# Optimization experiments

Measured on AMD Instinct MI355X. Metric: run time of the kernel, lower is better.

The kernel has to match this reference:

```python
import jax, jax.numpy as jnp
import numpy as np


def setup_inputs() -> dict:
    key = jax.random.key(0)
    k1, k2 = jax.random.split(key)
    B, D, K = 8192, 4096, 16
    x = jax.random.normal(k1, (B, D), dtype=jnp.float32)
    # kaiming_uniform_(a=sqrt(5)) on [K, D]: bound = sqrt(6/((1+5)*fan_in)) = 1/sqrt(D)
    bound = 1.0 / np.sqrt(D)
    w = jax.random.uniform(k2, (K, D), dtype=jnp.float32, minval=-bound, maxval=bound)
    return {"x": x, "w": w}


def reference(x, w):
    # z[b,d] = x[b,d] * (1 + sum_{i=1..k} w[i-1,d] * x[b,(d+i) mod D])
    k = w.shape[0]
    acc = jnp.ones_like(x)
    for i in range(1, k + 1):
        acc = acc + w[i - 1][None, :] * jnp.roll(x, -i, axis=1)
    return x * acc
```

## Files before the change

kernel.cpp:

```cpp
#include <hip/hip_runtime.h>


#define D 4096
#define DG 1024
#define K 16
#define TPB 256
#define RPB 16

typedef float f32x4 __attribute__((ext_vector_type(4)));

__global__ __launch_bounds__(TPB) void quad_enhancer_kernel(
    const float* __restrict__ x, const float* __restrict__ w,
    float* __restrict__ out) {
  const int tid = threadIdx.x;
  const int cg = blockIdx.x * TPB + tid;
  const int b0 = blockIdx.y * RPB;

  const float4* __restrict__ x4 = (const float4*)x;
  const float4* __restrict__ w4 = (const float4*)w;
  f32x4* __restrict__ o4 = (f32x4*)out;

  const int g1 = (cg + 1) & (DG - 1);
  const int g2 = (cg + 2) & (DG - 1);
  const int g3 = (cg + 3) & (DG - 1);
  const int g4 = (cg + 4) & (DG - 1);

  float4 wv[K];
#pragma unroll
  for (int i = 0; i < K; ++i) wv[i] = w4[i * DG + cg];
#pragma unroll
  for (int i = 0; i < K; ++i) {
    asm volatile("" : "+v"(wv[i].x), "+v"(wv[i].y), "+v"(wv[i].z),
                      "+v"(wv[i].w));
  }

  auto loadrow = [&](int r, float4* buf) {
    const float4* __restrict__ xr = x4 + (size_t)(b0 + r) * DG;
    buf[0] = xr[cg];
    buf[1] = xr[g1];
    buf[2] = xr[g2];
    buf[3] = xr[g3];
    buf[4] = xr[g4];
  };

  auto compute_store = [&](int r, const float4* buf) {
    float xs[20];
#pragma unroll
    for (int j = 0; j < 5; ++j) {
      xs[4 * j + 0] = buf[j].x;
      xs[4 * j + 1] = buf[j].y;
      xs[4 * j + 2] = buf[j].z;
      xs[4 * j + 3] = buf[j].w;
    }
    float ax = 1.0f, ay = 1.0f, az = 1.0f, aw = 1.0f;
#pragma unroll
    for (int i = 0; i < K; ++i) {
      ax = fmaf(wv[i].x, xs[i + 1], ax);
      ay = fmaf(wv[i].y, xs[i + 2], ay);
      az = fmaf(wv[i].z, xs[i + 3], az);
      aw = fmaf(wv[i].w, xs[i + 4], aw);
    }
    f32x4 o;
    o.x = xs[0] * ax;
    o.y = xs[1] * ay;
    o.z = xs[2] * az;
    o.w = xs[3] * aw;
    __builtin_nontemporal_store(o, &o4[(size_t)(b0 + r) * DG + cg]);
  };

  float4 A[5], B[5];
  loadrow(0, A);
#pragma unroll
  for (int r = 0; r < RPB; r += 2) {
    loadrow(r + 1, B);
    compute_store(r, A);
    if (r + 2 < RPB) loadrow(r + 2, A);
    compute_store(r + 1, B);
  }
}

extern "C" void kernel_launch(void* const* d_in, const int* in_sizes, int n_in,
                              void* d_out, int out_size, void* d_ws, size_t ws_size,
                              hipStream_t stream) {
  const float* x = (const float*)d_in[0];
  const float* w = (const float*)d_in[1];
  float* out = (float*)d_out;
  const int B = in_sizes[0] / D;

  dim3 grid(DG / TPB, B / RPB);
  quad_enhancer_kernel<<<grid, TPB, 0, stream>>>(x, w, out);
}
```

Baseline: 277.7 us.

## Replace manual double-buffered row pipeline with rolled loop over more rows

Doubles rows per block and replaces the hand double-buffered, fully unrolled row pipeline with a non-unrolled loop that loads, computes and stores one row per iteration, advancing row pointers. The compiler barrier on the weights is moved inside the loop so they stay pinned in registers. This cuts code size and register pressure and amortises the weight loads over more rows. The cost is losing explicit load/compute overlap within a thread and halving the grid size.

Result: slower. 322.6 us (+16.2%).

```diff
diff --git a/kernel.cpp b/kernel.cpp
--- a/kernel.cpp
+++ b/kernel.cpp
@@ -5,7 +5,7 @@
 #define DG 1024
 #define K 16
 #define TPB 256
-#define RPB 16
+#define RPB 32
 
 typedef float f32x4 __attribute__((ext_vector_type(4)));
 
@@ -28,30 +28,31 @@
   float4 wv[K];
 #pragma unroll
   for (int i = 0; i < K; ++i) wv[i] = w4[i * DG + cg];
+
+  const float4* __restrict__ xr = x4 + (size_t)b0 * DG;
+  f32x4* __restrict__ orow = o4 + (size_t)b0 * DG;
+
+#pragma unroll 1
+  for (int r = 0; r < RPB; ++r) {
 #pragma unroll
-  for (int i = 0; i < K; ++i) {
-    asm volatile("" : "+v"(wv[i].x), "+v"(wv[i].y), "+v"(wv[i].z),
-                      "+v"(wv[i].w));
-  }
+    for (int i = 0; i < K; ++i) {
+      asm volatile("" : "+v"(wv[i].x), "+v"(wv[i].y), "+v"(wv[i].z),
+                        "+v"(wv[i].w));
+    }
 
-  auto loadrow = [&](int r, float4* buf) {
-    const float4* __restrict__ xr = x4 + (size_t)(b0 + r) * DG;
-    buf[0] = xr[cg];
-    buf[1] = xr[g1];
-    buf[2] = xr[g2];
-    buf[3] = xr[g3];
-    buf[4] = xr[g4];
-  };
+    float4 v0 = xr[cg];
+    float4 v1 = xr[g1];
+    float4 v2 = xr[g2];
+    float4 v3 = xr[g3];
+    float4 v4 = xr[g4];
 
-  auto compute_store = [&](int r, const float4* buf) {
     float xs[20];
-#pragma unroll
-    for (int j = 0; j < 5; ++j) {
-      xs[4 * j + 0] = buf[j].x;
-      xs[4 * j + 1] = buf[j].y;
-      xs[4 * j + 2] = buf[j].z;
-      xs[4 * j + 3] = buf[j].w;
-    }
+    xs[0] = v0.x;  xs[1] = v0.y;  xs[2] = v0.z;  xs[3] = v0.w;
+    xs[4] = v1.x;  xs[5] = v1.y;  xs[6] = v1.z;  xs[7] = v1.w;
+    xs[8] = v2.x;  xs[9] = v2.y;  xs[10] = v2.z; xs[11] = v2.w;
+    xs[12] = v3.x; xs[13] = v3.y; xs[14] = v3.z; xs[15] = v3.w;
+    xs[16] = v4.x; xs[17] = v4.y; xs[18] = v4.z; xs[19] = v4.w;
+
     float ax = 1.0f, ay = 1.0f, az = 1.0f, aw = 1.0f;
 #pragma unroll
     for (int i = 0; i < K; ++i) {
@@ -60,22 +61,16 @@
       az = fmaf(wv[i].z, xs[i + 3], az);
       aw = fmaf(wv[i].w, xs[i + 4], aw);
     }
+
     f32x4 o;
     o.x = xs[0] * ax;
     o.y = xs[1] * ay;
     o.z = xs[2] * az;
     o.w = xs[3] * aw;
-    __builtin_nontemporal_store(o, &o4[(size_t)(b0 + r) * DG + cg]);
-  };
+    __builtin_nontemporal_store(o, &orow[cg]);
 
-  float4 A[5], B[5];
-  loadrow(0, A);
-#pragma unroll
-  for (int r = 0; r < RPB; r += 2) {
-    loadrow(r + 1, B);
-    compute_store(r, A);
-    if (r + 2 < RPB) loadrow(r + 2, A);
-    compute_store(r + 1, B);
+    xr += DG;
+    orow += DG;
   }
 }
 
```
